# Optimization experiments

Measured on AMD Instinct MI355X. Metric: run time of the kernel, lower is better.

Reference implementation:

```python
import jax, jax.numpy as jnp
import numpy as np

N_NODES = 50000


def _sage_conv(x, src, dst, Wl, bl, Wr):
    # mean aggregation of neighbor (source) features at destination nodes
    msg = x[src]                                              # [E, d]
    agg = jax.ops.segment_sum(msg, dst, num_segments=N_NODES)  # [N, d]
    cnt = jax.ops.segment_sum(jnp.ones((src.shape[0],), x.dtype), dst,
                              num_segments=N_NODES)            # [N]
    agg = agg / jnp.clip(cnt, 1.0)[:, None]
    # lin_l(aggregated) + lin_r(self), bias only on lin_l (PyG default)
    return agg @ Wl + bl + x @ Wr


def setup_inputs() -> dict:
    key = jax.random.key(0)
    ks = jax.random.split(key, 8)
    d = 128
    E = 800000
    x = jax.random.normal(ks[0], (N_NODES, d), dtype=jnp.float32)
    edge_index = jax.random.randint(ks[1], (2, E), 0, N_NODES, dtype=jnp.int64)
    s1 = 1.0 / np.sqrt(d)
    s2 = 1.0 / np.sqrt(32)
    return {
        "x": x,
        "edge_index": edge_index,
        "W1l": jax.random.normal(ks[2], (d, 32), jnp.float32) * s1,
        "b1": jnp.zeros((32,), jnp.float32),
        "W1r": jax.random.normal(ks[3], (d, 32), jnp.float32) * s1,
        "W2l": jax.random.normal(ks[4], (32, 32), jnp.float32) * s2,
        "b2": jnp.zeros((32,), jnp.float32),
        "W2r": jax.random.normal(ks[5], (32, 32), jnp.float32) * s2,
    }


def reference(x, edge_index, W1l, b1, W1r, W2l, b2, W2r):
    src, dst = edge_index[0], edge_index[1]
    h = jax.nn.relu(_sage_conv(x, src, dst, W1l, b1, W1r))
    return _sage_conv(h, src, dst, W2l, b2, W2r)
```

## Files before the change

kernel.cpp:

```cpp
#include <hip/hip_runtime.h>


#define N_NODES 50000
#define NB 782
#define BKS 64
#define GB 256
#define CAPE 1280
#define TILE 3200

__global__ __launch_bounds__(256) void k_front(
    const float* __restrict__ in, const float* __restrict__ Wl,
    const float* __restrict__ Wr, float* __restrict__ zl,
    float* __restrict__ zr, int N, int K, const int* __restrict__ src,
    const int* __restrict__ dst, int* __restrict__ gcnt,
    int* __restrict__ ebuf, int E) {
  __shared__ __align__(16) union {
    struct { float xs[64 * 68]; float ws[64 * 64]; } p;
    struct { unsigned pe[TILE]; int hist[NB]; int cur[NB]; } b;
  } sm;
  const int t = threadIdx.x;

  if (blockIdx.x < GB) {
    const int chunk = (((E + GB - 1) / GB) + 3) & ~3;
    const int e0 = blockIdx.x * chunk;
    int e1 = e0 + chunk;
    if (e1 > E) e1 = E;
    for (int ts = e0; ts < e1; ts += TILE) {
      int te = ts + TILE;
      if (te > e1) te = e1;
      const int n = te - ts;
      if (n <= 0) break;
      for (int i = t; i < NB; i += 256) sm.b.hist[i] = 0;
      __syncthreads();
      {
        const int n4 = n >> 2;
        const int4* s4 = (const int4*)(src + ts);
        const int4* d4 = (const int4*)(dst + ts);
        for (int i = t; i < n4; i += 256) {
          int4 sv = s4[i];
          int4 dv = d4[i];
          int4 pk;
          pk.x = (sv.x << 16) | dv.x;
          pk.y = (sv.y << 16) | dv.y;
          pk.z = (sv.z << 16) | dv.z;
          pk.w = (sv.w << 16) | dv.w;
          *(int4*)(sm.b.pe + 4 * i) = pk;
          atomicAdd(&sm.b.hist[dv.x >> 6], 1);
          atomicAdd(&sm.b.hist[dv.y >> 6], 1);
          atomicAdd(&sm.b.hist[dv.z >> 6], 1);
          atomicAdd(&sm.b.hist[dv.w >> 6], 1);
        }
        for (int i = (n4 << 2) + t; i < n; i += 256) {
          unsigned s = (unsigned)src[ts + i];
          unsigned d = (unsigned)dst[ts + i];
          sm.b.pe[i] = (s << 16) | d;
          atomicAdd(&sm.b.hist[d >> 6], 1);
        }
      }
      __syncthreads();
      for (int c = t; c < NB; c += 256) {
        int h = sm.b.hist[c];
        sm.b.cur[c] = h ? atomicAdd(&gcnt[c * 32], h) : 0;
      }
      __syncthreads();
      for (int i = t; i < n; i += 256) {
        unsigned pe = sm.b.pe[i];
        int d = (int)(pe & 0xFFFFu);
        int s = (int)(pe >> 16);
        int c = d >> 6;
        int p = atomicAdd(&sm.b.cur[c], 1);
        if (p < CAPE) ebuf[(size_t)c * CAPE + p] = (s << 6) | (d & 63);
      }
      __syncthreads();
    }
    return;
  }

  const int n0 = (blockIdx.x - GB) * 64;
  const int nvalid = (N - n0) < 64 ? (N - n0) : 64;
  const int tx = t & 15, ty = t >> 4;
  const int c0 = tx * 4;
  const int nl = ty * 4;

  float acc[4][4];
#pragma unroll
  for (int i = 0; i < 4; i++)
#pragma unroll
    for (int j = 0; j < 4; j++) acc[i][j] = 0.f;

  for (int kc = 0; kc < K; kc += 64) {
    const int KC = (K - kc) < 64 ? (K - kc) : 64;
    for (int i = t; i < KC * 32; i += 256) {
      int k = i >> 5, c = i & 31;
      sm.p.ws[k * 64 + c] = Wl[(size_t)(kc + k) * 32 + c];
      sm.p.ws[k * 64 + 32 + c] = Wr[(size_t)(kc + k) * 32 + c];
    }
    {
      const int kq = KC >> 2;
      const int sh = (KC == 64) ? 4 : 3;
      const int lim = nvalid * kq;
      for (int i = t; i < lim; i += 256) {
        int n = i >> sh, q = i & (kq - 1);
        float4 v = *(const float4*)(in + (size_t)(n0 + n) * K + kc + q * 4);
        *(float4*)(sm.p.xs + n * 68 + q * 4) = v;
      }
    }
    __syncthreads();

    const float* x0 = sm.p.xs + (nl + 0) * 68;
    const float* x1 = sm.p.xs + (nl + 1) * 68;
    const float* x2 = sm.p.xs + (nl + 2) * 68;
    const float* x3 = sm.p.xs + (nl + 3) * 68;
    for (int k = 0; k < KC; k += 4) {
      float4 xa = *(const float4*)(x0 + k);
      float4 xb = *(const float4*)(x1 + k);
      float4 xc = *(const float4*)(x2 + k);
      float4 xd = *(const float4*)(x3 + k);
#pragma unroll
      for (int kk = 0; kk < 4; kk++) {
        float4 w = *(const float4*)(sm.p.ws + (k + kk) * 64 + c0);
        float va = ((const float*)&xa)[kk];
        float vb = ((const float*)&xb)[kk];
        float vc = ((const float*)&xc)[kk];
        float vd = ((const float*)&xd)[kk];
        acc[0][0] += va * w.x; acc[0][1] += va * w.y;
        acc[0][2] += va * w.z; acc[0][3] += va * w.w;
        acc[1][0] += vb * w.x; acc[1][1] += vb * w.y;
        acc[1][2] += vb * w.z; acc[1][3] += vb * w.w;
        acc[2][0] += vc * w.x; acc[2][1] += vc * w.y;
        acc[2][2] += vc * w.z; acc[2][3] += vc * w.w;
        acc[3][0] += vd * w.x; acc[3][1] += vd * w.y;
        acc[3][2] += vd * w.z; acc[3][3] += vd * w.w;
      }
    }
    __syncthreads();
  }
#pragma unroll
  for (int i = 0; i < 4; i++) {
    int node = n0 + nl + i;
    if (node < N) {
      float4 v = make_float4(acc[i][0], acc[i][1], acc[i][2], acc[i][3]);
      if (c0 < 32)
        *(float4*)(zl + (size_t)node * 32 + c0) = v;
      else
        *(float4*)(zr + (size_t)node * 32 + (c0 - 32)) = v;
    }
  }
}

__global__ __launch_bounds__(256) void k_sort(int* __restrict__ ebuf,
                                              const int* __restrict__ gcnt,
                                              int2* __restrict__ nod, int N) {
  __shared__ __align__(16) int lds_e[CAPE];
  __shared__ int lds_s[CAPE];
  __shared__ int deg[BKS];
  __shared__ int cur[BKS];
  __shared__ int off[BKS];
  const int t = threadIdx.x;
  const int k = blockIdx.x;
  int ne = gcnt[k * 32];
  if (ne > CAPE) ne = CAPE;
  const size_t base = (size_t)k * CAPE;

  {
    const int ne4 = ne >> 2;
    const int4* eb4 = (const int4*)(ebuf + base);
    for (int i = t; i < ne4; i += 256) *(int4*)(lds_e + 4 * i) = eb4[i];
    for (int i = (ne4 << 2) + t; i < ne; i += 256) lds_e[i] = ebuf[base + i];
  }
  if (t < BKS) deg[t] = 0;
  __syncthreads();
  for (int i = t; i < ne; i += 256) atomicAdd(&deg[lds_e[i] & 63], 1);
  __syncthreads();
  if (t < 64) {
    int d = deg[t];
    int x = d;
#pragma unroll
    for (int o = 1; o < 64; o <<= 1) {
      int y = __shfl_up(x, o, 64);
      if (t >= o) x += y;
    }
    off[t] = x - d;
    cur[t] = x - d;
  }
  __syncthreads();
  for (int i = t; i < ne; i += 256) {
    int v = lds_e[i];
    int p = atomicAdd(&cur[v & 63], 1);
    lds_s[p] = v >> 6;
  }
  __syncthreads();
  for (int i = t; i < ne; i += 256) ebuf[base + i] = lds_s[i];
  if (t < BKS) {
    int node = (k << 6) + t;
    if (node < N) nod[node] = make_int2((int)base + off[t], deg[t]);
  }
}

__global__ __launch_bounds__(512) void k_fagg1(
    const float* __restrict__ zl, const float* __restrict__ zr,
    const int* __restrict__ adj, const int2* __restrict__ nod,
    const float* __restrict__ b1, const float* __restrict__ W2l,
    const float* __restrict__ W2r, float* __restrict__ z2l,
    float* __restrict__ z2r, int N) {
  __shared__ float w2p[32 * 64];
  __shared__ __align__(16) float bsh[32];
  __shared__ __align__(16) float hbuf[BKS * 36];
  const int t = threadIdx.x;
  const int k = blockIdx.x;
  for (int i = t; i < 2048; i += 512) {
    int jj = i >> 6, c = i & 63;
    w2p[i] = (c < 32) ? W2l[jj * 32 + c] : W2r[jj * 32 + (c - 32)];
  }
  if (t < 32) bsh[t] = b1[t];
  __syncthreads();

  const int g = t >> 3, fi = t & 7;
  const int node = (k << 6) + g;
  if (node < N) {
    const int2 nd = nod[node];
    const float4* zl4 = (const float4*)zl;
    float4 acc = make_float4(0.f, 0.f, 0.f, 0.f);
    for (int b0 = 0; b0 < nd.y; b0 += 8) {
      const int myi = b0 + fi;
      int sidx = (myi < nd.y) ? adj[nd.x + myi] : 0;
#pragma unroll
      for (int q = 0; q < 8; q++) {
        if (b0 + q < nd.y) {
          int s = __shfl(sidx, q, 8);
          float4 f = zl4[(size_t)s * 8 + fi];
          acc.x += f.x; acc.y += f.y; acc.z += f.z; acc.w += f.w;
        }
      }
    }
    const float rd = 1.0f / (float)(nd.y > 1 ? nd.y : 1);
    const float4 b4 = *(const float4*)(bsh + fi * 4);
    const float4 sA = *(const float4*)(zr + (size_t)node * 32 + fi * 4);
    float4 h;
    h.x = fmaxf(acc.x * rd + b4.x + sA.x, 0.f);
    h.y = fmaxf(acc.y * rd + b4.y + sA.y, 0.f);
    h.z = fmaxf(acc.z * rd + b4.z + sA.z, 0.f);
    h.w = fmaxf(acc.w * rd + b4.w + sA.w, 0.f);
    *(float4*)(hbuf + g * 36 + fi * 4) = h;
  }
  __syncthreads();

  const int gg = t >> 5, j = t & 31;
  const int n0 = k << 6;
#pragma unroll
  for (int i = 0; i < 4; i++) {
    const int nl = gg * 4 + i;
    const int nodei = n0 + nl;
    if (nodei >= N) break;
    const float h = hbuf[nl * 36 + j];
    float p0 = 0.f, p1 = 0.f;
#pragma unroll
    for (int jj = 0; jj < 32; jj++) {
      float hj = __shfl(h, jj, 32);
      p0 += hj * w2p[jj * 64 + j];
      p1 += hj * w2p[jj * 64 + 32 + j];
    }
    z2l[(size_t)nodei * 32 + j] = p0;
    z2r[(size_t)nodei * 32 + j] = p1;
  }
}

__global__ __launch_bounds__(256) void k_fagg2(
    const float* __restrict__ z2l, const float* __restrict__ z2r,
    const int* __restrict__ adj, const int2* __restrict__ nod,
    const float* __restrict__ b2, float* __restrict__ out, int N) {
  __shared__ __align__(16) float bsh[32];
  const int t = threadIdx.x;
  if (t < 32) bsh[t] = b2[t];
  __syncthreads();
  const int g = t >> 3, fi = t & 7;
  const int node = blockIdx.x * 32 + g;
  if (node >= N) return;
  const int2 nd = nod[node];
  const float4* z24 = (const float4*)z2l;
  float4 acc = make_float4(0.f, 0.f, 0.f, 0.f);
  for (int b0 = 0; b0 < nd.y; b0 += 8) {
    const int myi = b0 + fi;
    int sidx = (myi < nd.y) ? adj[nd.x + myi] : 0;
#pragma unroll
    for (int q = 0; q < 8; q++) {
      if (b0 + q < nd.y) {
        int s = __shfl(sidx, q, 8);
        float4 f = z24[(size_t)s * 8 + fi];
        acc.x += f.x; acc.y += f.y; acc.z += f.z; acc.w += f.w;
      }
    }
  }
  const float rd = 1.0f / (float)(nd.y > 1 ? nd.y : 1);
  const float4 b4 = *(const float4*)(bsh + fi * 4);
  const float4 sB = *(const float4*)(z2r + (size_t)node * 32 + fi * 4);
  float4 o;
  o.x = acc.x * rd + b4.x + sB.x;
  o.y = acc.y * rd + b4.y + sB.y;
  o.z = acc.z * rd + b4.z + sB.z;
  o.w = acc.w * rd + b4.w + sB.w;
  *(float4*)(out + (size_t)node * 32 + fi * 4) = o;
}

extern "C" void kernel_launch(void* const* d_in, const int* in_sizes, int n_in,
                              void* d_out, int out_size, void* d_ws,
                              size_t ws_size, hipStream_t stream) {
  const float* x = (const float*)d_in[0];
  const int* ei = (const int*)d_in[1];
  const float* W1l = (const float*)d_in[2];
  const float* b1 = (const float*)d_in[3];
  const float* W1r = (const float*)d_in[4];
  const float* W2l = (const float*)d_in[5];
  const float* b2 = (const float*)d_in[6];
  const float* W2r = (const float*)d_in[7];
  float* out = (float*)d_out;

  const int N = N_NODES;
  const int E = in_sizes[1] / 2;

  float* zl = (float*)d_ws;
  float* zr = zl + (size_t)N * 32;
  float* z2l = zr + (size_t)N * 32;
  float* z2r = z2l + (size_t)N * 32;
  int* ebuf = (int*)(z2r + (size_t)N * 32);
  int* gcnt = ebuf + (size_t)NB * CAPE;
  int2* nod = (int2*)(gcnt + (size_t)NB * 32);

  const int* srcp = ei;
  const int* dstp = ei + E;

  const int nblk_proj = (N + 63) / 64;
  const int nblk_f2 = (N + 31) / 32;

  hipMemsetAsync(gcnt, 0, (size_t)NB * 32 * sizeof(int), stream);
  k_front<<<GB + nblk_proj, 256, 0, stream>>>(x, W1l, W1r, zl, zr, N, 128,
                                              srcp, dstp, gcnt, ebuf, E);
  k_sort<<<NB, 256, 0, stream>>>(ebuf, gcnt, nod, N);
  k_fagg1<<<NB, 512, 0, stream>>>(zl, zr, ebuf, nod, b1, W2l, W2r, z2l, z2r,
                                  N);
  k_fagg2<<<nblk_f2, 256, 0, stream>>>(z2l, z2r, ebuf, nod, b2, out, N);
}
```

Measured before the change: 166.8 us.

## Fuse all stages into one persistent kernel with software grid barriers

Replaces the four kernel launches (front, sort, layer-1 aggregate, layer-2 aggregate) with a single persistent kernel of 1024 blocks that separates phases with atomic-counter grid barriers. Each block bins one edge chunk and computes one projection tile, then runs the sort, fused aggregate-plus-projection and final aggregation phases. This removes launch gaps and inter-kernel drain, at the cost of barrier spin time, fewer threads per block in the layer-1 phase, and a deadlock risk if all 1024 blocks cannot be co-resident.

```diff
diff --git a/kernel.cpp b/kernel.cpp
--- a/kernel.cpp
+++ b/kernel.cpp
@@ -4,58 +4,75 @@
 #define N_NODES 50000
 #define NB 782
 #define BKS 64
-#define GB 256
 #define CAPE 1280
-#define TILE 3200
-
-__global__ __launch_bounds__(256) void k_front(
-    const float* __restrict__ in, const float* __restrict__ Wl,
-    const float* __restrict__ Wr, float* __restrict__ zl,
-    float* __restrict__ zr, int N, int K, const int* __restrict__ src,
-    const int* __restrict__ dst, int* __restrict__ gcnt,
-    int* __restrict__ ebuf, int E) {
+#define GRID 1024
+
+typedef unsigned int u32;
+
+__device__ __forceinline__ void gridbar(u32* bar, u32 target) {
+  __syncthreads();
+  if (threadIdx.x == 0) {
+    __hip_atomic_fetch_add(bar, 1u, __ATOMIC_RELEASE,
+                           __HIP_MEMORY_SCOPE_AGENT);
+    while (__hip_atomic_load(bar, __ATOMIC_ACQUIRE,
+                             __HIP_MEMORY_SCOPE_AGENT) < target)
+      __builtin_amdgcn_s_sleep(16);
+  }
+  __syncthreads();
+}
+
+__global__ __launch_bounds__(256, 4) void k_all(
+    const float* __restrict__ x, const int* __restrict__ src,
+    const int* __restrict__ dst, const float* __restrict__ W1l,
+    const float* __restrict__ b1, const float* __restrict__ W1r,
+    const float* __restrict__ W2l, const float* __restrict__ b2,
+    const float* __restrict__ W2r, float* __restrict__ zl,
+    float* __restrict__ zr, float* __restrict__ z2l,
+    float* __restrict__ z2r, int* __restrict__ ebuf, int* __restrict__ gcnt,
+    u32* __restrict__ bar, int2* __restrict__ nod, float* __restrict__ out,
+    int N, int E) {
   __shared__ __align__(16) union {
     struct { float xs[64 * 68]; float ws[64 * 64]; } p;
-    struct { unsigned pe[TILE]; int hist[NB]; int cur[NB]; } b;
+    struct { unsigned pe[800]; int hist[NB]; int cur[NB]; } b;
+    struct { int e[CAPE]; int s[CAPE]; int deg[BKS]; int cur[BKS];
+             int off[BKS]; } s;
+    struct { float w2p[32 * 64]; float bsh[32]; float hbuf[BKS * 36]; } f;
   } sm;
   const int t = threadIdx.x;
-
-  if (blockIdx.x < GB) {
-    const int chunk = (((E + GB - 1) / GB) + 3) & ~3;
-    const int e0 = blockIdx.x * chunk;
+  const int bid = blockIdx.x;
+  const u32 G = gridDim.x;
+
+  {
+    const int chunk = (((E + GRID - 1) / GRID) + 3) & ~3;
+    const int e0 = bid * chunk;
     int e1 = e0 + chunk;
     if (e1 > E) e1 = E;
-    for (int ts = e0; ts < e1; ts += TILE) {
-      int te = ts + TILE;
-      if (te > e1) te = e1;
-      const int n = te - ts;
-      if (n <= 0) break;
+    const int n = e1 - e0;
+    if (n > 0) {
       for (int i = t; i < NB; i += 256) sm.b.hist[i] = 0;
       __syncthreads();
-      {
-        const int n4 = n >> 2;
-        const int4* s4 = (const int4*)(src + ts);
-        const int4* d4 = (const int4*)(dst + ts);
-        for (int i = t; i < n4; i += 256) {
-          int4 sv = s4[i];
-          int4 dv = d4[i];
-          int4 pk;
-          pk.x = (sv.x << 16) | dv.x;
-          pk.y = (sv.y << 16) | dv.y;
-          pk.z = (sv.z << 16) | dv.z;
-          pk.w = (sv.w << 16) | dv.w;
-          *(int4*)(sm.b.pe + 4 * i) = pk;
-          atomicAdd(&sm.b.hist[dv.x >> 6], 1);
-          atomicAdd(&sm.b.hist[dv.y >> 6], 1);
-          atomicAdd(&sm.b.hist[dv.z >> 6], 1);
-          atomicAdd(&sm.b.hist[dv.w >> 6], 1);
-        }
-        for (int i = (n4 << 2) + t; i < n; i += 256) {
-          unsigned s = (unsigned)src[ts + i];
-          unsigned d = (unsigned)dst[ts + i];
-          sm.b.pe[i] = (s << 16) | d;
-          atomicAdd(&sm.b.hist[d >> 6], 1);
-        }
+      const int n4 = n >> 2;
+      const int4* s4 = (const int4*)(src + e0);
+      const int4* d4 = (const int4*)(dst + e0);
+      for (int i = t; i < n4; i += 256) {
+        int4 sv = s4[i];
+        int4 dv = d4[i];
+        int4 pk;
+        pk.x = (sv.x << 16) | dv.x;
+        pk.y = (sv.y << 16) | dv.y;
+        pk.z = (sv.z << 16) | dv.z;
+        pk.w = (sv.w << 16) | dv.w;
+        *(int4*)(sm.b.pe + 4 * i) = pk;
+        atomicAdd(&sm.b.hist[dv.x >> 6], 1);
+        atomicAdd(&sm.b.hist[dv.y >> 6], 1);
+        atomicAdd(&sm.b.hist[dv.z >> 6], 1);
+        atomicAdd(&sm.b.hist[dv.w >> 6], 1);
+      }
+      for (int i = (n4 << 2) + t; i < n; i += 256) {
+        unsigned s_ = (unsigned)src[e0 + i];
+        unsigned d_ = (unsigned)dst[e0 + i];
+        sm.b.pe[i] = (s_ << 16) | d_;
+        atomicAdd(&sm.b.hist[d_ >> 6], 1);
       }
       __syncthreads();
       for (int c = t; c < NB; c += 256) {
@@ -65,241 +82,227 @@
       __syncthreads();
       for (int i = t; i < n; i += 256) {
         unsigned pe = sm.b.pe[i];
-        int d = (int)(pe & 0xFFFFu);
-        int s = (int)(pe >> 16);
-        int c = d >> 6;
+        int d_ = (int)(pe & 0xFFFFu);
+        int s_ = (int)(pe >> 16);
+        int c = d_ >> 6;
         int p = atomicAdd(&sm.b.cur[c], 1);
-        if (p < CAPE) ebuf[(size_t)c * CAPE + p] = (s << 6) | (d & 63);
-      }
-      __syncthreads();
-    }
-    return;
-  }
-
-  const int n0 = (blockIdx.x - GB) * 64;
-  const int nvalid = (N - n0) < 64 ? (N - n0) : 64;
-  const int tx = t & 15, ty = t >> 4;
-  const int c0 = tx * 4;
-  const int nl = ty * 4;
-
-  float acc[4][4];
-#pragma unroll
-  for (int i = 0; i < 4; i++)
-#pragma unroll
-    for (int j = 0; j < 4; j++) acc[i][j] = 0.f;
-
-  for (int kc = 0; kc < K; kc += 64) {
-    const int KC = (K - kc) < 64 ? (K - kc) : 64;
-    for (int i = t; i < KC * 32; i += 256) {
-      int k = i >> 5, c = i & 31;
-      sm.p.ws[k * 64 + c] = Wl[(size_t)(kc + k) * 32 + c];
-      sm.p.ws[k * 64 + 32 + c] = Wr[(size_t)(kc + k) * 32 + c];
-    }
+        if (p < CAPE) ebuf[(size_t)c * CAPE + p] = (s_ << 6) | (d_ & 63);
+      }
+    }
+    __syncthreads();
+  }
+
+  if (bid < (N + 63) / 64) {
+    const int K = 128;
+    const int n0 = bid * 64;
+    const int nvalid = (N - n0) < 64 ? (N - n0) : 64;
+    const int tx = t & 15, ty = t >> 4;
+    const int c0 = tx * 4;
+    const int nl = ty * 4;
+
+    float acc[4][4];
+#pragma unroll
+    for (int i = 0; i < 4; i++)
+#pragma unroll
+      for (int j = 0; j < 4; j++) acc[i][j] = 0.f;
+
+    for (int kc = 0; kc < K; kc += 64) {
+      for (int i = t; i < 64 * 32; i += 256) {
+        int k = i >> 5, c = i & 31;
+        sm.p.ws[k * 64 + c] = W1l[(size_t)(kc + k) * 32 + c];
+        sm.p.ws[k * 64 + 32 + c] = W1r[(size_t)(kc + k) * 32 + c];
+      }
+      {
+        const int lim = nvalid * 16;
+        for (int i = t; i < lim; i += 256) {
+          int n = i >> 4, q = i & 15;
+          float4 v = *(const float4*)(x + (size_t)(n0 + n) * K + kc + q * 4);
+          *(float4*)(sm.p.xs + n * 68 + q * 4) = v;
+        }
+      }
+      __syncthreads();
+
+      const float* x0 = sm.p.xs + (nl + 0) * 68;
+      const float* x1 = sm.p.xs + (nl + 1) * 68;
+      const float* x2 = sm.p.xs + (nl + 2) * 68;
+      const float* x3 = sm.p.xs + (nl + 3) * 68;
+      for (int k = 0; k < 64; k += 4) {
+        float4 xa = *(const float4*)(x0 + k);
+        float4 xb = *(const float4*)(x1 + k);
+        float4 xc = *(const float4*)(x2 + k);
+        float4 xd = *(const float4*)(x3 + k);
+#pragma unroll
+        for (int kk = 0; kk < 4; kk++) {
+          float4 w = *(const float4*)(sm.p.ws + (k + kk) * 64 + c0);
+          float va = ((const float*)&xa)[kk];
+          float vb = ((const float*)&xb)[kk];
+          float vc = ((const float*)&xc)[kk];
+          float vd = ((const float*)&xd)[kk];
+          acc[0][0] += va * w.x; acc[0][1] += va * w.y;
+          acc[0][2] += va * w.z; acc[0][3] += va * w.w;
+          acc[1][0] += vb * w.x; acc[1][1] += vb * w.y;
+          acc[1][2] += vb * w.z; acc[1][3] += vb * w.w;
+          acc[2][0] += vc * w.x; acc[2][1] += vc * w.y;
+          acc[2][2] += vc * w.z; acc[2][3] += vc * w.w;
+          acc[3][0] += vd * w.x; acc[3][1] += vd * w.y;
+          acc[3][2] += vd * w.z; acc[3][3] += vd * w.w;
+        }
+      }
+      __syncthreads();
+    }
+#pragma unroll
+    for (int i = 0; i < 4; i++) {
+      int node = n0 + nl + i;
+      if (node < N) {
+        float4 v = make_float4(acc[i][0], acc[i][1], acc[i][2], acc[i][3]);
+        if (c0 < 32)
+          *(float4*)(zl + (size_t)node * 32 + c0) = v;
+        else
+          *(float4*)(zr + (size_t)node * 32 + (c0 - 32)) = v;
+      }
+    }
+  }
+
+  gridbar(bar, G);
+
+  if (bid < NB) {
+    int ne = gcnt[bid * 32];
+    if (ne > CAPE) ne = CAPE;
+    const size_t base = (size_t)bid * CAPE;
     {
-      const int kq = KC >> 2;
-      const int sh = (KC == 64) ? 4 : 3;
-      const int lim = nvalid * kq;
-      for (int i = t; i < lim; i += 256) {
-        int n = i >> sh, q = i & (kq - 1);
-        float4 v = *(const float4*)(in + (size_t)(n0 + n) * K + kc + q * 4);
-        *(float4*)(sm.p.xs + n * 68 + q * 4) = v;
-      }
-    }
-    __syncthreads();
-
-    const float* x0 = sm.p.xs + (nl + 0) * 68;
-    const float* x1 = sm.p.xs + (nl + 1) * 68;
-    const float* x2 = sm.p.xs + (nl + 2) * 68;
-    const float* x3 = sm.p.xs + (nl + 3) * 68;
-    for (int k = 0; k < KC; k += 4) {
-      float4 xa = *(const float4*)(x0 + k);
-      float4 xb = *(const float4*)(x1 + k);
-      float4 xc = *(const float4*)(x2 + k);
-      float4 xd = *(const float4*)(x3 + k);
-#pragma unroll
-      for (int kk = 0; kk < 4; kk++) {
-        float4 w = *(const float4*)(sm.p.ws + (k + kk) * 64 + c0);
-        float va = ((const float*)&xa)[kk];
-        float vb = ((const float*)&xb)[kk];
-        float vc = ((const float*)&xc)[kk];
-        float vd = ((const float*)&xd)[kk];
-        acc[0][0] += va * w.x; acc[0][1] += va * w.y;
-        acc[0][2] += va * w.z; acc[0][3] += va * w.w;
-        acc[1][0] += vb * w.x; acc[1][1] += vb * w.y;
-        acc[1][2] += vb * w.z; acc[1][3] += vb * w.w;
-        acc[2][0] += vc * w.x; acc[2][1] += vc * w.y;
-        acc[2][2] += vc * w.z; acc[2][3] += vc * w.w;
-        acc[3][0] += vd * w.x; acc[3][1] += vd * w.y;
-        acc[3][2] += vd * w.z; acc[3][3] += vd * w.w;
-      }
-    }
-    __syncthreads();
-  }
-#pragma unroll
-  for (int i = 0; i < 4; i++) {
-    int node = n0 + nl + i;
-    if (node < N) {
-      float4 v = make_float4(acc[i][0], acc[i][1], acc[i][2], acc[i][3]);
-      if (c0 < 32)
-        *(float4*)(zl + (size_t)node * 32 + c0) = v;
-      else
-        *(float4*)(zr + (size_t)node * 32 + (c0 - 32)) = v;
-    }
-  }
-}
-
-__global__ __launch_bounds__(256) void k_sort(int* __restrict__ ebuf,
-                                              const int* __restrict__ gcnt,
-                                              int2* __restrict__ nod, int N) {
-  __shared__ __align__(16) int lds_e[CAPE];
-  __shared__ int lds_s[CAPE];
-  __shared__ int deg[BKS];
-  __shared__ int cur[BKS];
-  __shared__ int off[BKS];
-  const int t = threadIdx.x;
-  const int k = blockIdx.x;
-  int ne = gcnt[k * 32];
-  if (ne > CAPE) ne = CAPE;
-  const size_t base = (size_t)k * CAPE;
+      const int ne4 = ne >> 2;
+      const int4* eb4 = (const int4*)(ebuf + base);
+      for (int i = t; i < ne4; i += 256) *(int4*)(sm.s.e + 4 * i) = eb4[i];
+      for (int i = (ne4 << 2) + t; i < ne; i += 256)
+        sm.s.e[i] = ebuf[base + i];
+    }
+    if (t < BKS) sm.s.deg[t] = 0;
+    __syncthreads();
+    for (int i = t; i < ne; i += 256) atomicAdd(&sm.s.deg[sm.s.e[i] & 63], 1);
+    __syncthreads();
+    if (t < 64) {
+      int d = sm.s.deg[t];
+      int xx = d;
+#pragma unroll
+      for (int o = 1; o < 64; o <<= 1) {
+        int y = __shfl_up(xx, o, 64);
+        if (t >= o) xx += y;
+      }
+      sm.s.off[t] = xx - d;
+      sm.s.cur[t] = xx - d;
+    }
+    __syncthreads();
+    for (int i = t; i < ne; i += 256) {
+      int v = sm.s.e[i];
+      int p = atomicAdd(&sm.s.cur[v & 63], 1);
+      sm.s.s[p] = v >> 6;
+    }
+    __syncthreads();
+    for (int i = t; i < ne; i += 256) ebuf[base + i] = sm.s.s[i];
+    if (t < BKS) {
+      int node = (bid << 6) + t;
+      if (node < N) nod[node] = make_int2((int)base + sm.s.off[t], sm.s.deg[t]);
+    }
+  }
+
+  gridbar(bar, 2 * G);
+
+  if (bid < NB) {
+    for (int i = t; i < 2048; i += 256) {
+      int jj = i >> 6, c = i & 63;
+      sm.f.w2p[i] = (c < 32) ? W2l[jj * 32 + c] : W2r[jj * 32 + (c - 32)];
+    }
+    if (t < 32) sm.f.bsh[t] = b1[t];
+    __syncthreads();
+
+    const int g = t >> 3, fi = t & 7;
+    const float4* zl4 = (const float4*)zl;
+#pragma unroll
+    for (int half = 0; half < 2; ++half) {
+      const int nl = g * 2 + half;
+      const int node = (bid << 6) + nl;
+      if (node < N) {
+        const int2 nd = nod[node];
+        float4 acc = make_float4(0.f, 0.f, 0.f, 0.f);
+        for (int b0 = 0; b0 < nd.y; b0 += 8) {
+          const int myi = b0 + fi;
+          int sidx = (myi < nd.y) ? ebuf[nd.x + myi] : 0;
+#pragma unroll
+          for (int q = 0; q < 8; q++) {
+            if (b0 + q < nd.y) {
+              int s_ = __shfl(sidx, q, 8);
+              float4 f = zl4[(size_t)s_ * 8 + fi];
+              acc.x += f.x; acc.y += f.y; acc.z += f.z; acc.w += f.w;
+            }
+          }
+        }
+        const float rd = 1.0f / (float)(nd.y > 1 ? nd.y : 1);
+        const float4 b4 = *(const float4*)(sm.f.bsh + fi * 4);
+        const float4 sA = *(const float4*)(zr + (size_t)node * 32 + fi * 4);
+        float4 h;
+        h.x = fmaxf(acc.x * rd + b4.x + sA.x, 0.f);
+        h.y = fmaxf(acc.y * rd + b4.y + sA.y, 0.f);
+        h.z = fmaxf(acc.z * rd + b4.z + sA.z, 0.f);
+        h.w = fmaxf(acc.w * rd + b4.w + sA.w, 0.f);
+        *(float4*)(sm.f.hbuf + nl * 36 + fi * 4) = h;
+      }
+    }
+    __syncthreads();
+
+    const int gg = t >> 5, j = t & 31;
+    const int n0 = bid << 6;
+#pragma unroll
+    for (int i = 0; i < 8; i++) {
+      const int nl = gg * 8 + i;
+      const int nodei = n0 + nl;
+      if (nodei >= N) break;
+      const float h = sm.f.hbuf[nl * 36 + j];
+      float p0 = 0.f, p1 = 0.f;
+#pragma unroll
+      for (int jj = 0; jj < 32; jj++) {
+        float hj = __shfl(h, jj, 32);
+        p0 += hj * sm.f.w2p[jj * 64 + j];
+        p1 += hj * sm.f.w2p[jj * 64 + 32 + j];
+      }
+      z2l[(size_t)nodei * 32 + j] = p0;
+      z2r[(size_t)nodei * 32 + j] = p1;
+    }
+  }
+
+  gridbar(bar, 3 * G);
 
   {
-    const int ne4 = ne >> 2;
-    const int4* eb4 = (const int4*)(ebuf + base);
-    for (int i = t; i < ne4; i += 256) *(int4*)(lds_e + 4 * i) = eb4[i];
-    for (int i = (ne4 << 2) + t; i < ne; i += 256) lds_e[i] = ebuf[base + i];
-  }
-  if (t < BKS) deg[t] = 0;
-  __syncthreads();
-  for (int i = t; i < ne; i += 256) atomicAdd(&deg[lds_e[i] & 63], 1);
-  __syncthreads();
-  if (t < 64) {
-    int d = deg[t];
-    int x = d;
-#pragma unroll
-    for (int o = 1; o < 64; o <<= 1) {
-      int y = __shfl_up(x, o, 64);
-      if (t >= o) x += y;
-    }
-    off[t] = x - d;
-    cur[t] = x - d;
-  }
-  __syncthreads();
-  for (int i = t; i < ne; i += 256) {
-    int v = lds_e[i];
-    int p = atomicAdd(&cur[v & 63], 1);
-    lds_s[p] = v >> 6;
-  }
-  __syncthreads();
-  for (int i = t; i < ne; i += 256) ebuf[base + i] = lds_s[i];
-  if (t < BKS) {
-    int node = (k << 6) + t;
-    if (node < N) nod[node] = make_int2((int)base + off[t], deg[t]);
-  }
-}
-
-__global__ __launch_bounds__(512) void k_fagg1(
-    const float* __restrict__ zl, const float* __restrict__ zr,
-    const int* __restrict__ adj, const int2* __restrict__ nod,
-    const float* __restrict__ b1, const float* __restrict__ W2l,
-    const float* __restrict__ W2r, float* __restrict__ z2l,
-    float* __restrict__ z2r, int N) {
-  __shared__ float w2p[32 * 64];
-  __shared__ __align__(16) float bsh[32];
-  __shared__ __align__(16) float hbuf[BKS * 36];
-  const int t = threadIdx.x;
-  const int k = blockIdx.x;
-  for (int i = t; i < 2048; i += 512) {
-    int jj = i >> 6, c = i & 63;
-    w2p[i] = (c < 32) ? W2l[jj * 32 + c] : W2r[jj * 32 + (c - 32)];
-  }
-  if (t < 32) bsh[t] = b1[t];
-  __syncthreads();
-
-  const int g = t >> 3, fi = t & 7;
-  const int node = (k << 6) + g;
-  if (node < N) {
-    const int2 nd = nod[node];
-    const float4* zl4 = (const float4*)zl;
-    float4 acc = make_float4(0.f, 0.f, 0.f, 0.f);
-    for (int b0 = 0; b0 < nd.y; b0 += 8) {
-      const int myi = b0 + fi;
-      int sidx = (myi < nd.y) ? adj[nd.x + myi] : 0;
-#pragma unroll
-      for (int q = 0; q < 8; q++) {
-        if (b0 + q < nd.y) {
-          int s = __shfl(sidx, q, 8);
-          float4 f = zl4[(size_t)s * 8 + fi];
-          acc.x += f.x; acc.y += f.y; acc.z += f.z; acc.w += f.w;
+    const int g = t >> 3, fi = t & 7;
+    const float4* z24 = (const float4*)z2l;
+    const float4 b4 = *(const float4*)(b2 + fi * 4);
+    for (int v = bid; v < (N + 31) / 32; v += (int)G) {
+      const int node = v * 32 + g;
+      if (node < N) {
+        const int2 nd = nod[node];
+        float4 acc = make_float4(0.f, 0.f, 0.f, 0.f);
+        for (int b0 = 0; b0 < nd.y; b0 += 8) {
+          const int myi = b0 + fi;
+          int sidx = (myi < nd.y) ? ebuf[nd.x + myi] : 0;
+#pragma unroll
+          for (int q = 0; q < 8; q++) {
+            if (b0 + q < nd.y) {
+              int s_ = __shfl(sidx, q, 8);
+              float4 f = z24[(size_t)s_ * 8 + fi];
+              acc.x += f.x; acc.y += f.y; acc.z += f.z; acc.w += f.w;
+            }
+          }
         }
-      }
-    }
-    const float rd = 1.0f / (float)(nd.y > 1 ? nd.y : 1);
-    const float4 b4 = *(const float4*)(bsh + fi * 4);
-    const float4 sA = *(const float4*)(zr + (size_t)node * 32 + fi * 4);
-    float4 h;
-    h.x = fmaxf(acc.x * rd + b4.x + sA.x, 0.f);
-    h.y = fmaxf(acc.y * rd + b4.y + sA.y, 0.f);
-    h.z = fmaxf(acc.z * rd + b4.z + sA.z, 0.f);
-    h.w = fmaxf(acc.w * rd + b4.w + sA.w, 0.f);
-    *(float4*)(hbuf + g * 36 + fi * 4) = h;
-  }
-  __syncthreads();
-
-  const int gg = t >> 5, j = t & 31;
-  const int n0 = k << 6;
-#pragma unroll
-  for (int i = 0; i < 4; i++) {
-    const int nl = gg * 4 + i;
-    const int nodei = n0 + nl;
-    if (nodei >= N) break;
-    const float h = hbuf[nl * 36 + j];
-    float p0 = 0.f, p1 = 0.f;
-#pragma unroll
-    for (int jj = 0; jj < 32; jj++) {
-      float hj = __shfl(h, jj, 32);
-      p0 += hj * w2p[jj * 64 + j];
-      p1 += hj * w2p[jj * 64 + 32 + j];
-    }
-    z2l[(size_t)nodei * 32 + j] = p0;
-    z2r[(size_t)nodei * 32 + j] = p1;
-  }
-}
-
-__global__ __launch_bounds__(256) void k_fagg2(
-    const float* __restrict__ z2l, const float* __restrict__ z2r,
-    const int* __restrict__ adj, const int2* __restrict__ nod,
-    const float* __restrict__ b2, float* __restrict__ out, int N) {
-  __shared__ __align__(16) float bsh[32];
-  const int t = threadIdx.x;
-  if (t < 32) bsh[t] = b2[t];
-  __syncthreads();
-  const int g = t >> 3, fi = t & 7;
-  const int node = blockIdx.x * 32 + g;
-  if (node >= N) return;
-  const int2 nd = nod[node];
-  const float4* z24 = (const float4*)z2l;
-  float4 acc = make_float4(0.f, 0.f, 0.f, 0.f);
-  for (int b0 = 0; b0 < nd.y; b0 += 8) {
-    const int myi = b0 + fi;
-    int sidx = (myi < nd.y) ? adj[nd.x + myi] : 0;
-#pragma unroll
-    for (int q = 0; q < 8; q++) {
-      if (b0 + q < nd.y) {
-        int s = __shfl(sidx, q, 8);
-        float4 f = z24[(size_t)s * 8 + fi];
-        acc.x += f.x; acc.y += f.y; acc.z += f.z; acc.w += f.w;
-      }
-    }
-  }
-  const float rd = 1.0f / (float)(nd.y > 1 ? nd.y : 1);
-  const float4 b4 = *(const float4*)(bsh + fi * 4);
-  const float4 sB = *(const float4*)(z2r + (size_t)node * 32 + fi * 4);
-  float4 o;
-  o.x = acc.x * rd + b4.x + sB.x;
-  o.y = acc.y * rd + b4.y + sB.y;
-  o.z = acc.z * rd + b4.z + sB.z;
-  o.w = acc.w * rd + b4.w + sB.w;
-  *(float4*)(out + (size_t)node * 32 + fi * 4) = o;
+        const float rd = 1.0f / (float)(nd.y > 1 ? nd.y : 1);
+        const float4 sB = *(const float4*)(z2r + (size_t)node * 32 + fi * 4);
+        float4 o;
+        o.x = acc.x * rd + b4.x + sB.x;
+        o.y = acc.y * rd + b4.y + sB.y;
+        o.z = acc.z * rd + b4.z + sB.z;
+        o.w = acc.w * rd + b4.w + sB.w;
+        *(float4*)(out + (size_t)node * 32 + fi * 4) = o;
+      }
+    }
+  }
 }
 
 extern "C" void kernel_launch(void* const* d_in, const int* in_sizes, int n_in,
@@ -324,19 +327,14 @@
   float* z2r = z2l + (size_t)N * 32;
   int* ebuf = (int*)(z2r + (size_t)N * 32);
   int* gcnt = ebuf + (size_t)NB * CAPE;
-  int2* nod = (int2*)(gcnt + (size_t)NB * 32);
+  u32* bar = (u32*)(gcnt + (size_t)NB * 32);
+  int2* nod = (int2*)(bar + 8);
 
   const int* srcp = ei;
   const int* dstp = ei + E;
 
-  const int nblk_proj = (N + 63) / 64;
-  const int nblk_f2 = (N + 31) / 32;
-
-  hipMemsetAsync(gcnt, 0, (size_t)NB * 32 * sizeof(int), stream);
-  k_front<<<GB + nblk_proj, 256, 0, stream>>>(x, W1l, W1r, zl, zr, N, 128,
-                                              srcp, dstp, gcnt, ebuf, E);
-  k_sort<<<NB, 256, 0, stream>>>(ebuf, gcnt, nod, N);
-  k_fagg1<<<NB, 512, 0, stream>>>(zl, zr, ebuf, nod, b1, W2l, W2r, z2l, z2r,
-                                  N);
-  k_fagg2<<<nblk_f2, 256, 0, stream>>>(z2l, z2r, ebuf, nod, b2, out, N);
+  hipMemsetAsync(gcnt, 0, ((size_t)NB * 32 + 8) * sizeof(int), stream);
+  k_all<<<GRID, 256, 0, stream>>>(x, srcp, dstp, W1l, b1, W1r, W2l, b2, W2r,
+                                  zl, zr, z2l, z2r, ebuf, gcnt, bar, nod, out,
+                                  N, E);
 }
```

After: 635.7 us. 3.81x slower.

## Split layer-1 aggregation from layer-2 projection into separate kernels

Applied to the files above, without the earlier changes.

The fused layer-1 aggregate plus layer-2 projection kernel is split in two. One kernel aggregates neighbors, applies bias and ReLU, and writes h into the output buffer. A new register-tiled kernel then computes the 32x64 projection from shared memory. This is meant to raise occupancy and give smaller blocks for the irregular gather. The cost is an extra launch and a round trip of h through global memory.

```diff
diff --git a/kernel.cpp b/kernel.cpp
--- a/kernel.cpp
+++ b/kernel.cpp
@@ -197,71 +197,113 @@
   }
 }
 
-__global__ __launch_bounds__(512) void k_fagg1(
+__global__ __launch_bounds__(256) void k_fagg1(
     const float* __restrict__ zl, const float* __restrict__ zr,
     const int* __restrict__ adj, const int2* __restrict__ nod,
-    const float* __restrict__ b1, const float* __restrict__ W2l,
-    const float* __restrict__ W2r, float* __restrict__ z2l,
+    const float* __restrict__ b1, float* __restrict__ h, int N) {
+  __shared__ __align__(16) float bsh[32];
+  const int t = threadIdx.x;
+  if (t < 32) bsh[t] = b1[t];
+  __syncthreads();
+  const int g = t >> 3, fi = t & 7;
+  const int node = blockIdx.x * 32 + g;
+  if (node >= N) return;
+  const int2 nd = nod[node];
+  const float4* zl4 = (const float4*)zl;
+  float4 acc = make_float4(0.f, 0.f, 0.f, 0.f);
+  for (int b0 = 0; b0 < nd.y; b0 += 8) {
+    const int myi = b0 + fi;
+    int sidx = (myi < nd.y) ? adj[nd.x + myi] : 0;
+#pragma unroll
+    for (int q = 0; q < 8; q++) {
+      if (b0 + q < nd.y) {
+        int s = __shfl(sidx, q, 8);
+        float4 f = zl4[(size_t)s * 8 + fi];
+        acc.x += f.x; acc.y += f.y; acc.z += f.z; acc.w += f.w;
+      }
+    }
+  }
+  const float rd = 1.0f / (float)(nd.y > 1 ? nd.y : 1);
+  const float4 b4 = *(const float4*)(bsh + fi * 4);
+  const float4 sA = *(const float4*)(zr + (size_t)node * 32 + fi * 4);
+  float4 o;
+  o.x = fmaxf(acc.x * rd + b4.x + sA.x, 0.f);
+  o.y = fmaxf(acc.y * rd + b4.y + sA.y, 0.f);
+  o.z = fmaxf(acc.z * rd + b4.z + sA.z, 0.f);
+  o.w = fmaxf(acc.w * rd + b4.w + sA.w, 0.f);
+  *(float4*)(h + (size_t)node * 32 + fi * 4) = o;
+}
+
+__global__ __launch_bounds__(256) void kproj2(
+    const float* __restrict__ h, const float* __restrict__ Wl,
+    const float* __restrict__ Wr, float* __restrict__ z2l,
     float* __restrict__ z2r, int N) {
-  __shared__ float w2p[32 * 64];
-  __shared__ __align__(16) float bsh[32];
-  __shared__ __align__(16) float hbuf[BKS * 36];
-  const int t = threadIdx.x;
-  const int k = blockIdx.x;
-  for (int i = t; i < 2048; i += 512) {
-    int jj = i >> 6, c = i & 63;
-    w2p[i] = (c < 32) ? W2l[jj * 32 + c] : W2r[jj * 32 + (c - 32)];
-  }
-  if (t < 32) bsh[t] = b1[t];
-  __syncthreads();
-
-  const int g = t >> 3, fi = t & 7;
-  const int node = (k << 6) + g;
-  if (node < N) {
-    const int2 nd = nod[node];
-    const float4* zl4 = (const float4*)zl;
-    float4 acc = make_float4(0.f, 0.f, 0.f, 0.f);
-    for (int b0 = 0; b0 < nd.y; b0 += 8) {
-      const int myi = b0 + fi;
-      int sidx = (myi < nd.y) ? adj[nd.x + myi] : 0;
-#pragma unroll
-      for (int q = 0; q < 8; q++) {
-        if (b0 + q < nd.y) {
-          int s = __shfl(sidx, q, 8);
-          float4 f = zl4[(size_t)s * 8 + fi];
-          acc.x += f.x; acc.y += f.y; acc.z += f.z; acc.w += f.w;
-        }
-      }
-    }
-    const float rd = 1.0f / (float)(nd.y > 1 ? nd.y : 1);
-    const float4 b4 = *(const float4*)(bsh + fi * 4);
-    const float4 sA = *(const float4*)(zr + (size_t)node * 32 + fi * 4);
-    float4 h;
-    h.x = fmaxf(acc.x * rd + b4.x + sA.x, 0.f);
-    h.y = fmaxf(acc.y * rd + b4.y + sA.y, 0.f);
-    h.z = fmaxf(acc.z * rd + b4.z + sA.z, 0.f);
-    h.w = fmaxf(acc.w * rd + b4.w + sA.w, 0.f);
-    *(float4*)(hbuf + g * 36 + fi * 4) = h;
-  }
-  __syncthreads();
-
-  const int gg = t >> 5, j = t & 31;
-  const int n0 = k << 6;
+  __shared__ __align__(16) float xs[64 * 36];
+  __shared__ __align__(16) float ws[32 * 64];
+  const int t = threadIdx.x;
+  const int n0 = blockIdx.x * 64;
+  const int nvalid = (N - n0) < 64 ? (N - n0) : 64;
+  const int tx = t & 15, ty = t >> 4;
+  const int c0 = tx * 4;
+  const int nl = ty * 4;
+
+  for (int i = t; i < 32 * 32; i += 256) {
+    int k = i >> 5, c = i & 31;
+    ws[k * 64 + c] = Wl[k * 32 + c];
+    ws[k * 64 + 32 + c] = Wr[k * 32 + c];
+  }
+  {
+    const int lim = nvalid * 8;
+    for (int i = t; i < lim; i += 256) {
+      int n = i >> 3, q = i & 7;
+      float4 v = *(const float4*)(h + (size_t)(n0 + n) * 32 + q * 4);
+      *(float4*)(xs + n * 36 + q * 4) = v;
+    }
+  }
+  __syncthreads();
+
+  float acc[4][4];
+#pragma unroll
+  for (int i = 0; i < 4; i++)
+#pragma unroll
+    for (int j = 0; j < 4; j++) acc[i][j] = 0.f;
+
+  const float* x0 = xs + (nl + 0) * 36;
+  const float* x1 = xs + (nl + 1) * 36;
+  const float* x2 = xs + (nl + 2) * 36;
+  const float* x3 = xs + (nl + 3) * 36;
+  for (int k = 0; k < 32; k += 4) {
+    float4 xa = *(const float4*)(x0 + k);
+    float4 xb = *(const float4*)(x1 + k);
+    float4 xc = *(const float4*)(x2 + k);
+    float4 xd = *(const float4*)(x3 + k);
+#pragma unroll
+    for (int kk = 0; kk < 4; kk++) {
+      float4 w = *(const float4*)(ws + (k + kk) * 64 + c0);
+      float va = ((const float*)&xa)[kk];
+      float vb = ((const float*)&xb)[kk];
+      float vc = ((const float*)&xc)[kk];
+      float vd = ((const float*)&xd)[kk];
+      acc[0][0] += va * w.x; acc[0][1] += va * w.y;
+      acc[0][2] += va * w.z; acc[0][3] += va * w.w;
+      acc[1][0] += vb * w.x; acc[1][1] += vb * w.y;
+      acc[1][2] += vb * w.z; acc[1][3] += vb * w.w;
+      acc[2][0] += vc * w.x; acc[2][1] += vc * w.y;
+      acc[2][2] += vc * w.z; acc[2][3] += vc * w.w;
+      acc[3][0] += vd * w.x; acc[3][1] += vd * w.y;
+      acc[3][2] += vd * w.z; acc[3][3] += vd * w.w;
+    }
+  }
 #pragma unroll
   for (int i = 0; i < 4; i++) {
-    const int nl = gg * 4 + i;
-    const int nodei = n0 + nl;
-    if (nodei >= N) break;
-    const float h = hbuf[nl * 36 + j];
-    float p0 = 0.f, p1 = 0.f;
-#pragma unroll
-    for (int jj = 0; jj < 32; jj++) {
-      float hj = __shfl(h, jj, 32);
-      p0 += hj * w2p[jj * 64 + j];
-      p1 += hj * w2p[jj * 64 + 32 + j];
-    }
-    z2l[(size_t)nodei * 32 + j] = p0;
-    z2r[(size_t)nodei * 32 + j] = p1;
+    int node = n0 + nl + i;
+    if (node < N) {
+      float4 v = make_float4(acc[i][0], acc[i][1], acc[i][2], acc[i][3]);
+      if (c0 < 32)
+        *(float4*)(z2l + (size_t)node * 32 + c0) = v;
+      else
+        *(float4*)(z2r + (size_t)node * 32 + (c0 - 32)) = v;
+    }
   }
 }
 
@@ -325,18 +367,19 @@
   int* ebuf = (int*)(z2r + (size_t)N * 32);
   int* gcnt = ebuf + (size_t)NB * CAPE;
   int2* nod = (int2*)(gcnt + (size_t)NB * 32);
+  float* h = out;
 
   const int* srcp = ei;
   const int* dstp = ei + E;
 
   const int nblk_proj = (N + 63) / 64;
-  const int nblk_f2 = (N + 31) / 32;
+  const int nblk_f = (N + 31) / 32;
 
   hipMemsetAsync(gcnt, 0, (size_t)NB * 32 * sizeof(int), stream);
   k_front<<<GB + nblk_proj, 256, 0, stream>>>(x, W1l, W1r, zl, zr, N, 128,
                                               srcp, dstp, gcnt, ebuf, E);
   k_sort<<<NB, 256, 0, stream>>>(ebuf, gcnt, nod, N);
-  k_fagg1<<<NB, 512, 0, stream>>>(zl, zr, ebuf, nod, b1, W2l, W2r, z2l, z2r,
-                                  N);
-  k_fagg2<<<nblk_f2, 256, 0, stream>>>(z2l, z2r, ebuf, nod, b2, out, N);
-}
+  k_fagg1<<<nblk_f, 256, 0, stream>>>(zl, zr, ebuf, nod, b1, h, N);
+  kproj2<<<nblk_proj, 256, 0, stream>>>(h, W2l, W2r, z2l, z2r, N);
+  k_fagg2<<<nblk_f, 256, 0, stream>>>(z2l, z2r, ebuf, nod, b2, out, N);
+}
```

New measurement: 160.3 us. -3.9%, faster.
